# Kernel optimization log

Measured on AMD Instinct MI355X. Metric: run time of the kernel, lower is better.

## Reference

```python
import jax, jax.numpy as jnp
import numpy as np

E = 256  # embedding_dim
H = 256  # hidden_dim
B = 65536


def setup_inputs() -> dict:
    key = jax.random.key(0)
    ks = jax.random.split(key, 15)
    inp = {
        "x": jax.random.normal(ks[0], (B, E), dtype=jnp.float32),
        "c": jax.random.normal(ks[1], (B, H), dtype=jnp.float32),
        "h": jax.random.normal(ks[2], (B, H), dtype=jnp.float32),
    }
    names = ["W_i", "U_i", "b_i", "W_f", "U_f", "b_f", "W_c", "U_c", "b_c", "W_o", "U_o", "b_o"]
    shapes = [(E, H), (H, H), (H,)] * 4
    for n, s, k in zip(names, shapes, ks[3:]):
        inp[n] = jax.random.normal(k, s, dtype=jnp.float32)
    return inp


def reference(x, c, h, W_i, U_i, b_i, W_f, U_f, b_f, W_c, U_c, b_c, W_o, U_o, b_o):
    # Batch the four input/hidden projections into two GEMMs, then fuse gates.
    W = jnp.concatenate([W_f, W_i, W_o, W_c], axis=1)  # [E, 4H]
    U = jnp.concatenate([U_f, U_i, U_o, U_c], axis=1)  # [H, 4H]
    b = jnp.concatenate([b_f, b_i, b_o, b_c], axis=0)  # [4H]
    z = x @ W + h @ U + b                               # [B, 4H]
    zf, zi, zo, zg = jnp.split(z, 4, axis=1)
    f = jax.nn.sigmoid(zf)
    i = jax.nn.sigmoid(zi)
    o = jax.nn.sigmoid(zo)
    g = jnp.tanh(zg)
    c_new = c * f + g * i
    h_new = o * jnp.tanh(c_new)
    return (c_new, h_new)
```

## Files before the change

### kernel.cpp

```cpp
#include <hip/hip_runtime.h>
#include <hip/hip_fp16.h>

typedef _Float16 half8 __attribute__((ext_vector_type(8)));
typedef float f32x4 __attribute__((ext_vector_type(4)));

#define BATCH 65536
#define KD 512
#define HD 256
#define BHSZ 16777216

__device__ __forceinline__ void gload16(const _Float16* g, _Float16* lds) {
  __builtin_amdgcn_global_load_lds((const __attribute__((address_space(1))) void*)g,
                                   (__attribute__((address_space(3))) void*)lds,
                                   16, 0, 0);
}

__device__ __forceinline__ float fast_sigmoid(float z) {
  float e = __builtin_amdgcn_exp2f(-z * 1.4426950408889634f);
  return __builtin_amdgcn_rcpf(1.0f + e);
}

__device__ __forceinline__ float fast_tanh(float z) {
  float a = __builtin_fabsf(z);
  float e = __builtin_amdgcn_exp2f(a * 2.8853900817779268f);
  float t = 1.0f - 2.0f * __builtin_amdgcn_rcpf(1.0f + e);
  return z < 0.0f ? -t : t;
}

__global__ __launch_bounds__(256) void pack_a(const float* __restrict__ x,
                                              const float* __restrict__ h,
                                              _Float16* __restrict__ A) {
  long i = (long)blockIdx.x * 256 + threadIdx.x;
  long e = i * 8;
  int b = (int)(e >> 9);
  int k = (int)(e & 511);
  const float* src = (k < 256) ? (x + (long)b * 256 + k)
                               : (h + (long)b * 256 + (k - 256));
  float4 v0 = reinterpret_cast<const float4*>(src)[0];
  float4 v1 = reinterpret_cast<const float4*>(src)[1];
  half8 o;
  o[0] = (_Float16)v0.x; o[1] = (_Float16)v0.y;
  o[2] = (_Float16)v0.z; o[3] = (_Float16)v0.w;
  o[4] = (_Float16)v1.x; o[5] = (_Float16)v1.y;
  o[6] = (_Float16)v1.z; o[7] = (_Float16)v1.w;
  *reinterpret_cast<half8*>(A + e) = o;
}

__global__ __launch_bounds__(256) void pack_b(
    const float* __restrict__ Wf, const float* __restrict__ Uf,
    const float* __restrict__ Wi, const float* __restrict__ Ui,
    const float* __restrict__ Wo, const float* __restrict__ Uo,
    const float* __restrict__ Wc, const float* __restrict__ Uc,
    _Float16* __restrict__ Bp) {
  int idx = blockIdx.x * 256 + threadIdx.x;
  int k = idx & 511;
  int Np = idx >> 9;
  int g = (Np >> 4) & 3;
  int cl = ((Np >> 6) << 4) | (Np & 15);
  const float* W;
  const float* U;
  switch (g) {
    case 0: W = Wf; U = Uf; break;
    case 1: W = Wi; U = Ui; break;
    case 2: W = Wo; U = Uo; break;
    default: W = Wc; U = Uc; break;
  }
  float v = (k < 256) ? W[k * 256 + cl] : U[(k - 256) * 256 + cl];
  Bp[idx] = (_Float16)v;
}

__global__ __launch_bounds__(256) void lstm_gemm(
    const _Float16* __restrict__ A, const _Float16* __restrict__ Bp,
    const float* __restrict__ cin,
    const float* __restrict__ bf_, const float* __restrict__ bi_,
    const float* __restrict__ bo_, const float* __restrict__ bc_,
    float* __restrict__ out) {
  __shared__ _Float16 As[128 * 64];
  __shared__ _Float16 Bs[128 * 64];

  int tid = threadIdx.x;
  int w = tid >> 6, l = tid & 63;
  int l15 = l & 15, lg = l >> 4;
  int bx = blockIdx.x;
  int bm = bx >> 3, bn = bx & 7;
  int wr = w >> 1, wc = w & 1;

  long gaOff[4], gbOff[4];
  int ldsOff[4];
#pragma unroll
  for (int i2 = 0; i2 < 4; ++i2) {
    int idx = i2 * 256 + tid;
    int row = idx >> 3, slot = idx & 7;
    int swz = slot ^ (row & 7);
    gaOff[i2] = (long)(bm * 128 + row) * 512 + swz * 8;
    gbOff[i2] = (long)(bn * 128 + row) * 512 + swz * 8;
    ldsOff[i2] = (i2 * 256 + w * 64) * 8;
  }

  f32x4 acc[4][4];
#pragma unroll
  for (int a2 = 0; a2 < 4; ++a2)
#pragma unroll
    for (int b2 = 0; b2 < 4; ++b2)
      acc[a2][b2] = (f32x4){0.f, 0.f, 0.f, 0.f};

  for (int kt = 0; kt < 8; ++kt) {
    int ko = kt * 64;
#pragma unroll
    for (int i2 = 0; i2 < 4; ++i2) {
      gload16(A + gaOff[i2] + ko, As + ldsOff[i2]);
      gload16(Bp + gbOff[i2] + ko, Bs + ldsOff[i2]);
    }
    __syncthreads();
#pragma unroll
    for (int kk = 0; kk < 2; ++kk) {
      half8 av[4], bv[4];
#pragma unroll
      for (int mf = 0; mf < 4; ++mf) {
        int row = wr * 64 + mf * 16 + l15;
        int swz = (kk * 4 + lg) ^ (row & 7);
        av[mf] = *reinterpret_cast<const half8*>(&As[row * 64 + swz * 8]);
      }
#pragma unroll
      for (int nf = 0; nf < 4; ++nf) {
        int row = wc * 64 + nf * 16 + l15;
        int swz = (kk * 4 + lg) ^ (row & 7);
        bv[nf] = *reinterpret_cast<const half8*>(&Bs[row * 64 + swz * 8]);
      }
#pragma unroll
      for (int mf = 0; mf < 4; ++mf)
#pragma unroll
        for (int nf = 0; nf < 4; ++nf)
          acc[mf][nf] = __builtin_amdgcn_mfma_f32_16x16x32_f16(
              av[mf], bv[nf], acc[mf][nf], 0, 0, 0);
    }
    __syncthreads();
  }

  int t = bn * 2 + wc;
  int col = t * 16 + l15;
  float vbf = bf_[col], vbi = bi_[col], vbo = bo_[col], vbc = bc_[col];
#pragma unroll
  for (int mf = 0; mf < 4; ++mf) {
#pragma unroll
    for (int r = 0; r < 4; ++r) {
      long row = (long)(bm * 128 + wr * 64 + mf * 16 + lg * 4 + r);
      float zf = acc[mf][0][r] + vbf;
      float zi = acc[mf][1][r] + vbi;
      float zo = acc[mf][2][r] + vbo;
      float zg = acc[mf][3][r] + vbc;
      float fg = fast_sigmoid(zf);
      float ig = fast_sigmoid(zi);
      float og = fast_sigmoid(zo);
      float gg = fast_tanh(zg);
      float cv = cin[row * 256 + col];
      float cn = cv * fg + gg * ig;
      float hn = og * fast_tanh(cn);
      out[row * 256 + col] = cn;
      out[BHSZ + row * 256 + col] = hn;
    }
  }
}

extern "C" void kernel_launch(void* const* d_in, const int* in_sizes, int n_in,
                              void* d_out, int out_size, void* d_ws, size_t ws_size,
                              hipStream_t stream) {
  const float* x  = (const float*)d_in[0];
  const float* c  = (const float*)d_in[1];
  const float* h  = (const float*)d_in[2];
  const float* Wi = (const float*)d_in[3];
  const float* Ui = (const float*)d_in[4];
  const float* bi = (const float*)d_in[5];
  const float* Wf = (const float*)d_in[6];
  const float* Uf = (const float*)d_in[7];
  const float* bf = (const float*)d_in[8];
  const float* Wc = (const float*)d_in[9];
  const float* Uc = (const float*)d_in[10];
  const float* bc = (const float*)d_in[11];
  const float* Wo = (const float*)d_in[12];
  const float* Uo = (const float*)d_in[13];
  const float* bo = (const float*)d_in[14];

  _Float16* A  = (_Float16*)d_ws;
  _Float16* Bp = (_Float16*)((char*)d_ws + (size_t)BATCH * KD * 2);

  pack_a<<<16384, 256, 0, stream>>>(x, h, A);
  pack_b<<<2048, 256, 0, stream>>>(Wf, Uf, Wi, Ui, Wo, Uo, Wc, Uc, Bp);
  lstm_gemm<<<4096, 256, 0, stream>>>(A, Bp, c, bf, bi, bo, bc, (float*)d_out);
}
```

Before: 169.8 us.

## Fuse fp32-to-fp16 A conversion into GEMM with double-buffered LDS pipeline

Drops the separate pack_a kernel. The GEMM now loads fp32 x and h directly into registers, converts them to fp16, and writes them into swizzled LDS. Both A and B tiles are double-buffered, so the next K tile is prefetched while MFMAs run on the current one. Workgroup IDs are remapped, and s_setprio is raised around the MFMA blocks. This avoids writing and re-reading the 64 MB fp16 A intermediate and one kernel launch, at the cost of more registers and LDS, which may lower occupancy. It also makes each of the 8 column blocks re-read and re-convert the fp32 A rows.

```diff
diff --git a/kernel.cpp b/kernel.cpp
--- a/kernel.cpp
+++ b/kernel.cpp
@@ -2,6 +2,7 @@
 #include <hip/hip_fp16.h>
 
 typedef _Float16 half8 __attribute__((ext_vector_type(8)));
+typedef _Float16 half4 __attribute__((ext_vector_type(4)));
 typedef float f32x4 __attribute__((ext_vector_type(4)));
 
 #define BATCH 65536
@@ -25,25 +26,6 @@
   float e = __builtin_amdgcn_exp2f(a * 2.8853900817779268f);
   float t = 1.0f - 2.0f * __builtin_amdgcn_rcpf(1.0f + e);
   return z < 0.0f ? -t : t;
-}
-
-__global__ __launch_bounds__(256) void pack_a(const float* __restrict__ x,
-                                              const float* __restrict__ h,
-                                              _Float16* __restrict__ A) {
-  long i = (long)blockIdx.x * 256 + threadIdx.x;
-  long e = i * 8;
-  int b = (int)(e >> 9);
-  int k = (int)(e & 511);
-  const float* src = (k < 256) ? (x + (long)b * 256 + k)
-                               : (h + (long)b * 256 + (k - 256));
-  float4 v0 = reinterpret_cast<const float4*>(src)[0];
-  float4 v1 = reinterpret_cast<const float4*>(src)[1];
-  half8 o;
-  o[0] = (_Float16)v0.x; o[1] = (_Float16)v0.y;
-  o[2] = (_Float16)v0.z; o[3] = (_Float16)v0.w;
-  o[4] = (_Float16)v1.x; o[5] = (_Float16)v1.y;
-  o[6] = (_Float16)v1.z; o[7] = (_Float16)v1.w;
-  *reinterpret_cast<half8*>(A + e) = o;
 }
 
 __global__ __launch_bounds__(256) void pack_b(
@@ -69,33 +51,38 @@
   Bp[idx] = (_Float16)v;
 }
 
-__global__ __launch_bounds__(256) void lstm_gemm(
-    const _Float16* __restrict__ A, const _Float16* __restrict__ Bp,
-    const float* __restrict__ cin,
+__global__ __launch_bounds__(256) void lstm_fused(
+    const float* __restrict__ x, const float* __restrict__ h,
+    const _Float16* __restrict__ Bp, const float* __restrict__ cin,
     const float* __restrict__ bf_, const float* __restrict__ bi_,
     const float* __restrict__ bo_, const float* __restrict__ bc_,
     float* __restrict__ out) {
-  __shared__ _Float16 As[128 * 64];
-  __shared__ _Float16 Bs[128 * 64];
+  __shared__ _Float16 As[2][128 * 64];
+  __shared__ _Float16 Bs[2][128 * 64];
 
   int tid = threadIdx.x;
   int w = tid >> 6, l = tid & 63;
   int l15 = l & 15, lg = l >> 4;
-  int bx = blockIdx.x;
-  int bm = bx >> 3, bn = bx & 7;
+
+  int bid = blockIdx.x;
+  int wgid = (bid & 7) * 512 + (bid >> 3);
+  int bm = wgid >> 3, bn = wgid & 7;
   int wr = w >> 1, wc = w & 1;
 
-  long gaOff[4], gbOff[4];
-  int ldsOff[4];
+  long gbOff[4];
+  int ldsB[4];
 #pragma unroll
   for (int i2 = 0; i2 < 4; ++i2) {
     int idx = i2 * 256 + tid;
     int row = idx >> 3, slot = idx & 7;
     int swz = slot ^ (row & 7);
-    gaOff[i2] = (long)(bm * 128 + row) * 512 + swz * 8;
     gbOff[i2] = (long)(bn * 128 + row) * 512 + swz * 8;
-    ldsOff[i2] = (i2 * 256 + w * 64) * 8;
-  }
+    ldsB[i2] = (i2 * 256 + w * 64) * 8;
+  }
+
+  int arow = tid >> 4;
+  int am = tid & 15;
+  float4 aReg[8];
 
   f32x4 acc[4][4];
 #pragma unroll
@@ -104,14 +91,44 @@
     for (int b2 = 0; b2 < 4; ++b2)
       acc[a2][b2] = (f32x4){0.f, 0.f, 0.f, 0.f};
 
+  auto issueA = [&](int kt) {
+    const float* src = (kt < 4) ? x : h;
+    int ko = (kt & 3) * 64;
+#pragma unroll
+    for (int j = 0; j < 8; ++j) {
+      long row = (long)(bm * 128 + j * 16 + arow);
+      aReg[j] = *reinterpret_cast<const float4*>(src + row * 256 + ko + am * 4);
+    }
+  };
+  auto issueB = [&](int kt, int buf) {
+    int ko = kt * 64;
+#pragma unroll
+    for (int i2 = 0; i2 < 4; ++i2)
+      gload16(Bp + gbOff[i2] + ko, &Bs[buf][0] + ldsB[i2]);
+  };
+  auto writeA = [&](int buf) {
+#pragma unroll
+    for (int j = 0; j < 8; ++j) {
+      int row = j * 16 + arow;
+      int off = row * 64 + (((am >> 1) ^ (row & 7)) << 3) + ((am & 1) << 2);
+      half4 o;
+      o[0] = (_Float16)aReg[j].x; o[1] = (_Float16)aReg[j].y;
+      o[2] = (_Float16)aReg[j].z; o[3] = (_Float16)aReg[j].w;
+      *reinterpret_cast<half4*>(&As[buf][off]) = o;
+    }
+  };
+
+  issueA(0);
+  issueB(0, 0);
+  writeA(0);
+  __syncthreads();
+
+  int buf = 0;
   for (int kt = 0; kt < 8; ++kt) {
-    int ko = kt * 64;
-#pragma unroll
-    for (int i2 = 0; i2 < 4; ++i2) {
-      gload16(A + gaOff[i2] + ko, As + ldsOff[i2]);
-      gload16(Bp + gbOff[i2] + ko, Bs + ldsOff[i2]);
-    }
-    __syncthreads();
+    if (kt < 7) {
+      issueA(kt + 1);
+      issueB(kt + 1, buf ^ 1);
+    }
 #pragma unroll
     for (int kk = 0; kk < 2; ++kk) {
       half8 av[4], bv[4];
@@ -119,22 +136,26 @@
       for (int mf = 0; mf < 4; ++mf) {
         int row = wr * 64 + mf * 16 + l15;
         int swz = (kk * 4 + lg) ^ (row & 7);
-        av[mf] = *reinterpret_cast<const half8*>(&As[row * 64 + swz * 8]);
+        av[mf] = *reinterpret_cast<const half8*>(&As[buf][row * 64 + swz * 8]);
       }
 #pragma unroll
       for (int nf = 0; nf < 4; ++nf) {
         int row = wc * 64 + nf * 16 + l15;
         int swz = (kk * 4 + lg) ^ (row & 7);
-        bv[nf] = *reinterpret_cast<const half8*>(&Bs[row * 64 + swz * 8]);
+        bv[nf] = *reinterpret_cast<const half8*>(&Bs[buf][row * 64 + swz * 8]);
       }
+      __builtin_amdgcn_s_setprio(1);
 #pragma unroll
       for (int mf = 0; mf < 4; ++mf)
 #pragma unroll
         for (int nf = 0; nf < 4; ++nf)
           acc[mf][nf] = __builtin_amdgcn_mfma_f32_16x16x32_f16(
               av[mf], bv[nf], acc[mf][nf], 0, 0, 0);
-    }
+      __builtin_amdgcn_s_setprio(0);
+    }
+    if (kt < 7) writeA(buf ^ 1);
     __syncthreads();
+    buf ^= 1;
   }
 
   int t = bn * 2 + wc;
@@ -181,10 +202,9 @@
   const float* Uo = (const float*)d_in[13];
   const float* bo = (const float*)d_in[14];
 
-  _Float16* A  = (_Float16*)d_ws;
-  _Float16* Bp = (_Float16*)((char*)d_ws + (size_t)BATCH * KD * 2);
-
-  pack_a<<<16384, 256, 0, stream>>>(x, h, A);
+  _Float16* Bp = (_Float16*)d_ws;
+
   pack_b<<<2048, 256, 0, stream>>>(Wf, Uf, Wi, Ui, Wo, Uo, Wc, Uc, Bp);
-  lstm_gemm<<<4096, 256, 0, stream>>>(A, Bp, c, bf, bi, bo, bc, (float*)d_out);
-}
+  lstm_fused<<<4096, 256, 0, stream>>>(x, h, Bp, c, bf, bi, bo, bc,
+                                       (float*)d_out);
+}
```

Measured after the change: 178.2 us. 5.0% more time.

## Enlarge GEMM tile to 256x256 with double-buffered LDS prefetch pipeline

Applied to the files above, without the earlier changes.

The GEMM kernel now uses 512-thread blocks computing 256x256 output tiles instead of 128x128, with 128KB of LDS split into two buffers. Global-to-LDS loads for the next K step are interleaved with MFMA work on the current buffer, there is one barrier per K step, s_setprio raises wave priority around MFMA bursts, and block IDs are remapped to group tiles for cache locality. This aims to hide global load latency and raise operand reuse per LDS byte, at the cost of more registers per thread, fewer blocks (1024), and lower occupancy.

```diff
diff --git a/kernel.cpp b/kernel.cpp
--- a/kernel.cpp
+++ b/kernel.cpp
@@ -4,12 +4,9 @@
 typedef _Float16 half8 __attribute__((ext_vector_type(8)));
 typedef float f32x4 __attribute__((ext_vector_type(4)));
 
-#define BATCH 65536
-#define KD 512
-#define HD 256
 #define BHSZ 16777216
 
-__device__ __forceinline__ void gload16(const _Float16* g, _Float16* lds) {
+__device__ __forceinline__ void gload16(const void* g, const void* lds) {
   __builtin_amdgcn_global_load_lds((const __attribute__((address_space(1))) void*)g,
                                    (__attribute__((address_space(3))) void*)lds,
                                    16, 0, 0);
@@ -29,7 +26,7 @@
 
 __global__ __launch_bounds__(256) void pack_a(const float* __restrict__ x,
                                               const float* __restrict__ h,
-                                              _Float16* __restrict__ A) {
+                                              _Float16* __restrict__ Apk) {
   long i = (long)blockIdx.x * 256 + threadIdx.x;
   long e = i * 8;
   int b = (int)(e >> 9);
@@ -43,7 +40,7 @@
   o[2] = (_Float16)v0.z; o[3] = (_Float16)v0.w;
   o[4] = (_Float16)v1.x; o[5] = (_Float16)v1.y;
   o[6] = (_Float16)v1.z; o[7] = (_Float16)v1.w;
-  *reinterpret_cast<half8*>(A + e) = o;
+  *reinterpret_cast<half8*>(Apk + e) = o;
 }
 
 __global__ __launch_bounds__(256) void pack_b(
@@ -69,82 +66,141 @@
   Bp[idx] = (_Float16)v;
 }
 
-__global__ __launch_bounds__(256) void lstm_gemm(
-    const _Float16* __restrict__ A, const _Float16* __restrict__ Bp,
+__global__ __launch_bounds__(512, 2) void lstm_gemm(
+    const _Float16* __restrict__ Apk, const _Float16* __restrict__ Bp,
     const float* __restrict__ cin,
     const float* __restrict__ bf_, const float* __restrict__ bi_,
     const float* __restrict__ bo_, const float* __restrict__ bc_,
     float* __restrict__ out) {
-  __shared__ _Float16 As[128 * 64];
-  __shared__ _Float16 Bs[128 * 64];
+  __shared__ __align__(16) char smem[131072];
 
   int tid = threadIdx.x;
   int w = tid >> 6, l = tid & 63;
   int l15 = l & 15, lg = l >> 4;
-  int bx = blockIdx.x;
-  int bm = bx >> 3, bn = bx & 7;
-  int wr = w >> 1, wc = w & 1;
-
-  long gaOff[4], gbOff[4];
-  int ldsOff[4];
-#pragma unroll
-  for (int i2 = 0; i2 < 4; ++i2) {
-    int idx = i2 * 256 + tid;
-    int row = idx >> 3, slot = idx & 7;
-    int swz = slot ^ (row & 7);
-    gaOff[i2] = (long)(bm * 128 + row) * 512 + swz * 8;
-    gbOff[i2] = (long)(bn * 128 + row) * 512 + swz * 8;
-    ldsOff[i2] = (i2 * 256 + w * 64) * 8;
-  }
-
-  f32x4 acc[4][4];
-#pragma unroll
-  for (int a2 = 0; a2 < 4; ++a2)
+  int wr = w >> 2, wcn = w & 3;
+
+  int bid = blockIdx.x;
+  int wg = (bid & 7) * 128 + (bid >> 3);
+  int bm = wg >> 2, bn = wg & 3;
+
+  int rpl = tid >> 3, s8 = tid & 7;
+  int i8 = s8 ^ (rpl & 7);
+  int rbase = 2 * rpl + (i8 >> 2);
+  int csrc = (i8 & 3) * 8;
+  long sA = ((long)bm * 256 + rbase) * 512 + csrc;
+  long sB = ((long)bn * 256 + rbase) * 512 + csrc;
+  int wb1k = w * 1024;
+
+  int offA[8], offB[4];
+#pragma unroll
+  for (int mf = 0; mf < 8; ++mf) {
+    int r = wr * 128 + mf * 16 + l15;
+    int rp = r >> 1;
+    offA[mf] = rp * 128 + (((((r & 1) << 2) | lg) ^ (rp & 7)) << 4);
+  }
+#pragma unroll
+  for (int nf = 0; nf < 4; ++nf) {
+    int r = wcn * 64 + nf * 16 + l15;
+    int rp = r >> 1;
+    offB[nf] = 32768 + rp * 128 + (((((r & 1) << 2) | lg) ^ (rp & 7)) << 4);
+  }
+
+  f32x4 acc[8][4];
+#pragma unroll
+  for (int a2 = 0; a2 < 8; ++a2)
 #pragma unroll
     for (int b2 = 0; b2 < 4; ++b2)
       acc[a2][b2] = (f32x4){0.f, 0.f, 0.f, 0.f};
 
+  auto stageA = [&](int ktn, int hf, char* dbuf) {
+    const _Float16* s0 = Apk + sA + (long)ktn * 64 + (long)hf * 128 * 512;
+    gload16(s0, dbuf + hf * 8192 + wb1k);
+    gload16(s0 + 32, dbuf + 16384 + hf * 8192 + wb1k);
+  };
+  auto stageB = [&](int ktn, int hf, char* dbuf) {
+    const _Float16* s0 = Bp + sB + (long)ktn * 64 + (long)hf * 128 * 512;
+    gload16(s0, dbuf + 32768 + hf * 8192 + wb1k);
+    gload16(s0 + 32, dbuf + 49152 + hf * 8192 + wb1k);
+  };
+
+  stageA(0, 0, smem);
+  stageA(0, 1, smem);
+  stageB(0, 0, smem);
+  stageB(0, 1, smem);
+
+#pragma unroll
   for (int kt = 0; kt < 8; ++kt) {
-    int ko = kt * 64;
-#pragma unroll
-    for (int i2 = 0; i2 < 4; ++i2) {
-      gload16(A + gaOff[i2] + ko, As + ldsOff[i2]);
-      gload16(Bp + gbOff[i2] + ko, Bs + ldsOff[i2]);
-    }
     __syncthreads();
-#pragma unroll
-    for (int kk = 0; kk < 2; ++kk) {
-      half8 av[4], bv[4];
-#pragma unroll
-      for (int mf = 0; mf < 4; ++mf) {
-        int row = wr * 64 + mf * 16 + l15;
-        int swz = (kk * 4 + lg) ^ (row & 7);
-        av[mf] = *reinterpret_cast<const half8*>(&As[row * 64 + swz * 8]);
-      }
-#pragma unroll
-      for (int nf = 0; nf < 4; ++nf) {
-        int row = wc * 64 + nf * 16 + l15;
-        int swz = (kk * 4 + lg) ^ (row & 7);
-        bv[nf] = *reinterpret_cast<const half8*>(&Bs[row * 64 + swz * 8]);
-      }
-#pragma unroll
-      for (int mf = 0; mf < 4; ++mf)
-#pragma unroll
-        for (int nf = 0; nf < 4; ++nf)
-          acc[mf][nf] = __builtin_amdgcn_mfma_f32_16x16x32_f16(
-              av[mf], bv[nf], acc[mf][nf], 0, 0, 0);
-    }
-    __syncthreads();
-  }
-
-  int t = bn * 2 + wc;
-  int col = t * 16 + l15;
+    const char* rb = smem + (kt & 1) * 65536;
+    char* wbuf = smem + ((kt + 1) & 1) * 65536;
+    half8 av[4], bv[4];
+
+    if (kt < 7) stageA(kt + 1, 0, wbuf);
+#pragma unroll
+    for (int nf = 0; nf < 4; ++nf)
+      bv[nf] = *reinterpret_cast<const half8*>(rb + offB[nf]);
+#pragma unroll
+    for (int q = 0; q < 4; ++q)
+      av[q] = *reinterpret_cast<const half8*>(rb + offA[q]);
+    __builtin_amdgcn_s_setprio(1);
+#pragma unroll
+    for (int q = 0; q < 4; ++q)
+#pragma unroll
+      for (int nf = 0; nf < 4; ++nf)
+        acc[q][nf] = __builtin_amdgcn_mfma_f32_16x16x32_f16(
+            av[q], bv[nf], acc[q][nf], 0, 0, 0);
+    __builtin_amdgcn_s_setprio(0);
+
+    if (kt < 7) stageA(kt + 1, 1, wbuf);
+#pragma unroll
+    for (int q = 0; q < 4; ++q)
+      av[q] = *reinterpret_cast<const half8*>(rb + offA[4 + q]);
+    __builtin_amdgcn_s_setprio(1);
+#pragma unroll
+    for (int q = 0; q < 4; ++q)
+#pragma unroll
+      for (int nf = 0; nf < 4; ++nf)
+        acc[4 + q][nf] = __builtin_amdgcn_mfma_f32_16x16x32_f16(
+            av[q], bv[nf], acc[4 + q][nf], 0, 0, 0);
+    __builtin_amdgcn_s_setprio(0);
+
+    if (kt < 7) stageB(kt + 1, 0, wbuf);
+#pragma unroll
+    for (int nf = 0; nf < 4; ++nf)
+      bv[nf] = *reinterpret_cast<const half8*>(rb + 16384 + offB[nf]);
+#pragma unroll
+    for (int q = 0; q < 4; ++q)
+      av[q] = *reinterpret_cast<const half8*>(rb + 16384 + offA[q]);
+    __builtin_amdgcn_s_setprio(1);
+#pragma unroll
+    for (int q = 0; q < 4; ++q)
+#pragma unroll
+      for (int nf = 0; nf < 4; ++nf)
+        acc[q][nf] = __builtin_amdgcn_mfma_f32_16x16x32_f16(
+            av[q], bv[nf], acc[q][nf], 0, 0, 0);
+    __builtin_amdgcn_s_setprio(0);
+
+    if (kt < 7) stageB(kt + 1, 1, wbuf);
+#pragma unroll
+    for (int q = 0; q < 4; ++q)
+      av[q] = *reinterpret_cast<const half8*>(rb + 16384 + offA[4 + q]);
+    __builtin_amdgcn_s_setprio(1);
+#pragma unroll
+    for (int q = 0; q < 4; ++q)
+#pragma unroll
+      for (int nf = 0; nf < 4; ++nf)
+        acc[4 + q][nf] = __builtin_amdgcn_mfma_f32_16x16x32_f16(
+            av[q], bv[nf], acc[4 + q][nf], 0, 0, 0);
+    __builtin_amdgcn_s_setprio(0);
+  }
+
+  int col = (bn * 4 + wcn) * 16 + l15;
   float vbf = bf_[col], vbi = bi_[col], vbo = bo_[col], vbc = bc_[col];
 #pragma unroll
-  for (int mf = 0; mf < 4; ++mf) {
+  for (int mf = 0; mf < 8; ++mf) {
 #pragma unroll
     for (int r = 0; r < 4; ++r) {
-      long row = (long)(bm * 128 + wr * 64 + mf * 16 + lg * 4 + r);
+      long row = (long)(bm * 256 + wr * 128 + mf * 16 + lg * 4 + r);
       float zf = acc[mf][0][r] + vbf;
       float zi = acc[mf][1][r] + vbi;
       float zo = acc[mf][2][r] + vbo;
@@ -181,10 +237,11 @@
   const float* Uo = (const float*)d_in[13];
   const float* bo = (const float*)d_in[14];
 
-  _Float16* A  = (_Float16*)d_ws;
-  _Float16* Bp = (_Float16*)((char*)d_ws + (size_t)BATCH * KD * 2);
-
-  pack_a<<<16384, 256, 0, stream>>>(x, h, A);
+  _Float16* Apk = (_Float16*)d_ws;
+  _Float16* Bp  = (_Float16*)((char*)d_ws + (size_t)65536 * 512 * 2);
+
+  pack_a<<<16384, 256, 0, stream>>>(x, h, Apk);
   pack_b<<<2048, 256, 0, stream>>>(Wf, Uf, Wi, Ui, Wo, Uo, Wc, Uc, Bp);
-  lstm_gemm<<<4096, 256, 0, stream>>>(A, Bp, c, bf, bi, bo, bc, (float*)d_out);
-}
+  lstm_gemm<<<1024, 512, 0, stream>>>(Apk, Bp, c, bf, bi, bo, bc,
+                                      (float*)d_out);
+}
```

Result: faster. 143.2 us (-15.6%).
